# Optimization experiments

Hardware: AMD Instinct MI355X
Metric: run time of the kernel (lower is better)

The kernel has to match this reference:

```python
import jax, jax.numpy as jnp
import numpy as np

NH, HD = 12, 64          # heads, head dim (d_model=768)
SC = HD ** -0.5          # both Attention and CA_Attention use head_dim**-0.5


def patchify(x, p1, p2):
    # 'b c (h p1) (w p2) -> b (h w) (p1 p2 c)'
    B, C, H, W = x.shape
    h, w = H // p1, W // p2
    x = x.reshape(B, C, h, p1, w, p2).transpose(0, 2, 4, 3, 5, 1)  # b h w p1 p2 c
    return x.reshape(B, h * w, p1 * p2 * C)


def unpatchify(x, h, w, p1, p2, c):
    # 'b (h w) (p1 p2 c) -> b c (h p1) (w p2)'
    B = x.shape[0]
    x = x.reshape(B, h, w, p1, p2, c).transpose(0, 5, 1, 3, 2, 4)
    return x.reshape(B, c, h * p1, w * p2)


def ln(x, g, b):
    m = x.mean(-1, keepdims=True)
    v = ((x - m) ** 2).mean(-1, keepdims=True)
    return (x - m) / jnp.sqrt(v + 1e-5) * g + b


def setup_inputs() -> dict:
    key = jax.random.key(0)
    specs = [
        ('img_feats', (2, 32, 112, 112, 80)), ('txt', (2, 77, 768)),
        ('pe_w_ax', (1120, 768)), ('pe_b_ax', (768,)),
        ('pe_w_sag', (1120, 768)), ('pe_b_sag', (768,)),
        ('pe_w_cor', (1568, 768)), ('pe_b_cor', (768,)),
        ('pos_ax', (1, 256, 768)), ('pos_sag', (1, 256, 768)), ('pos_cor', (1, 256, 768)),
        ('qw', (768, 768)), ('kw', (768, 768)), ('vw', (768, 768)),
        ('pw', (768, 768)), ('pb', (768,)),
        ('caq_w', (768, 768)), ('caq_b', (768,)), ('cak_w', (768, 768)), ('cak_b', (768,)),
        ('cav_w', (768, 768)), ('cav_b', (768,)), ('cao_w', (768, 768)), ('cao_b', (768,)),
        ('mlp_w1', (768, 3072)), ('mlp_b1', (3072,)), ('mlp_w2', (3072, 768)), ('mlp_b2', (768,)),
        ('ow_ax', (768, 1120)), ('ob_ax', (1120,)),
        ('ow_sag', (768, 1120)), ('ob_sag', (1120,)),
        ('ow_cor', (768, 1568)), ('ob_cor', (1568,)),
    ]
    big = {'img_feats', 'txt', 'pos_ax', 'pos_sag', 'pos_cor'}
    out = {}
    for k, (n, s) in zip(jax.random.split(key, len(specs)), specs):
        scale = 1.0 if n in big else 0.02
        out[n] = jax.random.normal(k, s, jnp.float32) * scale
    out['view_w'] = jnp.ones((3,), jnp.float32)
    for n in ('n1_g', 'n2_g', 'n3_g'):
        out[n] = jnp.ones((768,), jnp.float32)
    for n in ('n1_b', 'n2_b', 'n3_b'):
        out[n] = jnp.zeros((768,), jnp.float32)
    return out


def reference(img_feats, txt, pe_w_ax, pe_b_ax, pe_w_sag, pe_b_sag, pe_w_cor, pe_b_cor,
              pos_ax, pos_sag, pos_cor, view_w, qw, kw, vw, pw, pb,
              caq_w, caq_b, cak_w, cak_b, cav_w, cav_b, cao_w, cao_b,
              n1_g, n1_b, n2_g, n2_b, n3_g, n3_b,
              mlp_w1, mlp_b1, mlp_w2, mlp_b2,
              ow_ax, ob_ax, ow_sag, ob_sag, ow_cor, ob_cor):

    def img_attn(t):
        B, N, C = t.shape
        q = (t @ qw).reshape(B, N, NH, HD)
        k = (t @ kw).reshape(B, N, NH, HD)
        v = (t @ vw).reshape(B, N, NH, HD)
        a = jax.nn.softmax(jnp.einsum('bnkc,bmkc->bknm', q, k) * SC, axis=-1)
        x = jnp.einsum('bknm,bmkc->bnkc', a, v).reshape(B, N, C)
        return x @ pw + pb

    def ca_attn(t, im):
        B, T, _ = t.shape
        N = im.shape[1]
        qh = (t @ caq_w + caq_b).reshape(B, T, NH, HD).transpose(0, 2, 1, 3)
        kh = (im @ cak_w + cak_b).reshape(B, N, NH, HD).transpose(0, 2, 1, 3)
        vh = (im @ cav_w + cav_b).reshape(B, N, NH, HD).transpose(0, 2, 1, 3)
        a = jax.nn.softmax(jnp.einsum('bhid,bhjd->bhij', qh, kh) * SC, axis=-1)
        # faithful to original einsum 'b h i j, b h j d -> b h j d' (sums over i)
        o = jnp.einsum('bhij,bhjd->bhjd', a, vh)
        o = o.transpose(0, 2, 1, 3).reshape(B, N, NH * HD)
        return o @ cao_w + cao_b

    def branch(v2d, pe_w, pe_b, pos, ow, ob, p1, p2):
        B, C, H, W = v2d.shape
        h, w = H // p1, W // p2
        q = patchify(v2d, p1, p2) @ pe_w + pe_b + pos
        q = ln(q, n1_g, n1_b)
        q = q + img_attn(q)
        q = ln(q, n2_g, n2_b)
        x = q + ca_attn(txt, q)
        x = x + (jax.nn.gelu(ln(x, n3_g, n3_b) @ mlp_w1 + mlp_b1, approximate=False) @ mlp_w2 + mlp_b2)
        return unpatchify(x @ ow + ob, h, w, p1, p2, C)

    # adaptive_avg_pool3d to size-1 along one axis == mean over that axis
    ax = img_feats.mean(2)    # (B,C,H,W)
    sag = img_feats.mean(3)   # (B,C,D,W)
    cor = img_feats.mean(4)   # (B,C,D,H)
    oax = branch(ax, pe_w_ax, pe_b_ax, pos_ax, ow_ax, ob_ax, 7, 5)
    osag = branch(sag, pe_w_sag, pe_b_sag, pos_sag, ow_sag, ob_sag, 7, 5)
    ocor = branch(cor, pe_w_cor, pe_b_cor, pos_cor, ow_cor, ob_cor, 7, 7)
    v3 = (view_w[0] * oax[:, :, None] + view_w[1] * osag[:, :, :, None]
          + view_w[2] * ocor[:, :, :, :, None])
    return img_feats + v3
```

## Files before the change

kernel.cpp:

```cpp
#include <hip/hip_runtime.h>
#include <math.h>

typedef __attribute__((ext_vector_type(8))) short s8;
typedef __attribute__((ext_vector_type(4))) float f4;
typedef unsigned short u16;

__device__ inline u16 f2bf(float f) {
    unsigned u = __float_as_uint(f);
    u += 0x7fffu + ((u >> 16) & 1u);
    return (u16)(u >> 16);
}
__device__ inline float bf2f(u16 x) {
    return __uint_as_float(((unsigned)x) << 16);
}

__global__ __launch_bounds__(256) void mean3_k(const float* __restrict__ img,
                                               float* __restrict__ axp,
                                               float* __restrict__ sag,
                                               float* __restrict__ cor) {
    __shared__ float sl[112*81];
    int blk = blockIdx.x;
    int dc = blk & 15, bc = blk >> 4;
    int d0 = dc * 7;
    int t = threadIdx.x;
    f4 axr[9];
    #pragma unroll
    for (int k = 0; k < 9; ++k) axr[k] = (f4){0.f,0.f,0.f,0.f};
    const float* base = img + (size_t)bc * 1003520 + (size_t)d0 * 8960;
    for (int sidx = 0; sidx < 7; ++sidx) {
        const f4* sp = reinterpret_cast<const f4*>(base + (size_t)sidx * 8960);
        #pragma unroll
        for (int k = 0; k < 9; ++k) {
            int q = t + k * 256;
            if (q < 2240) {
                f4 v = sp[q];
                axr[k] += v;
                int h = q / 20, w4 = q % 20;
                float* row = &sl[h * 81 + w4 * 4];
                row[0] = v[0]; row[1] = v[1]; row[2] = v[2]; row[3] = v[3];
            }
        }
        __syncthreads();
        if (t < 112) {
            float acc = 0.f;
            #pragma unroll 8
            for (int w = 0; w < 80; ++w) acc += sl[t * 81 + w];
            cor[((size_t)bc * 112 + d0 + sidx) * 112 + t] = acc * (1.f / 80.f);
        } else if (t < 192) {
            int w = t - 112;
            float acc = 0.f;
            #pragma unroll 8
            for (int h = 0; h < 112; ++h) acc += sl[h * 81 + w];
            sag[((size_t)bc * 112 + d0 + sidx) * 80 + w] = acc * (1.f / 112.f);
        }
        __syncthreads();
    }
    float* axo = axp + ((size_t)dc * 64 + bc) * 8960;
    #pragma unroll
    for (int k = 0; k < 9; ++k) {
        int q = t + k * 256;
        if (q < 2240) *reinterpret_cast<f4*>(axo + q * 4) = axr[k];
    }
}

__global__ void axred_k(const float* __restrict__ axp, float* __restrict__ ax) {
    int idx = blockIdx.x * 256 + threadIdx.x;
    if (idx >= 143360) return;
    f4 s = (f4){0.f,0.f,0.f,0.f};
    #pragma unroll
    for (int i = 0; i < 16; ++i)
        s += *reinterpret_cast<const f4*>(axp + (size_t)i * 573440 + (size_t)idx * 4);
    s *= (1.f / 112.f);
    *reinterpret_cast<f4*>(ax + (size_t)idx * 4) = s;
}

struct TT {
    const float* in[16];
    u16* out[16];
    int K[16];
    int N[16];
    int start[16];
};

__global__ __launch_bounds__(256) void transp_all(TT tab) {
    __shared__ float tl[32][33];
    int bid = blockIdx.x;
    int e = 0;
    #pragma unroll
    for (int i = 1; i < 16; ++i) if (bid >= tab.start[i]) e = i;
    const float* in = tab.in[e];
    u16* out = tab.out[e];
    int K = tab.K[e], N = tab.N[e];
    int tid = bid - tab.start[e];
    int nt = N >> 5;
    int k0 = (tid / nt) * 32, n0 = (tid % nt) * 32;
    int t = threadIdx.x;
    int r = t >> 5, c = t & 31;
    #pragma unroll
    for (int i = 0; i < 4; ++i) tl[r + i*8][c] = in[(long)(k0 + r + i*8)*N + n0 + c];
    __syncthreads();
    #pragma unroll
    for (int i = 0; i < 4; ++i) out[(long)(n0 + r + i*8)*K + k0 + c] = f2bf(tl[c][r + i*8]);
}

__global__ void misc_k(const float* __restrict__ txt, u16* __restrict__ txtb,
                       const float* __restrict__ cak_b, const float* __restrict__ cav_b,
                       float* __restrict__ kvb) {
    int idx = blockIdx.x*256 + threadIdx.x;
    if (idx < 118272) { txtb[idx] = f2bf(txt[idx]); return; }
    int i2 = idx - 118272;
    if (i2 < 768) kvb[i2] = cak_b[i2];
    else if (i2 < 1536) kvb[i2] = cav_b[i2 - 768];
}

__global__ __launch_bounds__(256) void patchify3_k(const float* __restrict__ m_ax,
                                                   const float* __restrict__ m_sag,
                                                   const float* __restrict__ m_cor,
                                                   u16* __restrict__ P0, u16* __restrict__ P1,
                                                   u16* __restrict__ P2) {
    __shared__ float sl[32][113];
    int br = blockIdx.y;
    int X = blockIdx.x;
    int b = X / 112, rem = X % 112;
    int hh = rem / 7, pp1 = rem % 7;
    const float* src; u16* dst; int Wt, p2, PD;
    if (br == 0)      { src = m_ax;  dst = P0; Wt = 80;  p2 = 5; PD = 1120; }
    else if (br == 1) { src = m_sag; dst = P1; Wt = 80;  p2 = 5; PD = 1120; }
    else              { src = m_cor; dst = P2; Wt = 112; p2 = 7; PD = 1568; }
    int t = threadIdx.x;
    int row = hh*7 + pp1;
    int wq = Wt >> 2;
    for (int i = t; i < 32*wq; i += 256) {
        int c = i / wq, w4 = i % wq;
        float4 v = *reinterpret_cast<const float4*>(
            src + ((size_t)(b*32 + c)*112 + row)*Wt + w4*4);
        sl[c][w4*4+0] = v.x; sl[c][w4*4+1] = v.y; sl[c][w4*4+2] = v.z; sl[c][w4*4+3] = v.w;
    }
    __syncthreads();
    int tot = 16 * p2 * 32;
    for (int o = t; o < tot; o += 256) {
        int ww = o / (p2*32), rest = o % (p2*32);
        int pp2 = rest >> 5, c = rest & 31;
        dst[((size_t)(b*256 + hh*16 + ww))*PD + (pp1*p2 + pp2)*32 + c]
            = f2bf(sl[c][ww*p2 + pp2]);
    }
}

__device__ inline void load_tile(const u16* __restrict__ P, int ld, int nrows, int K,
                                 int r0, int k0, int t, s8 v[4]) {
    #pragma unroll
    for (int i = 0; i < 4; ++i) {
        int chunk = t + i*256;
        int row = chunk >> 4, c8 = (chunk & 15) * 8;
        s8 x;
        #pragma unroll
        for (int q = 0; q < 8; ++q) x[q] = 0;
        if (r0 + row < nrows && k0 + c8 < K)
            x = *reinterpret_cast<const s8*>(P + (long)(r0 + row)*ld + k0 + c8);
        v[i] = x;
    }
}
__device__ inline void write_tile(u16 (*S)[136], int t, const s8 v[4]) {
    #pragma unroll
    for (int i = 0; i < 4; ++i) {
        int chunk = t + i*256;
        *reinterpret_cast<s8*>(&S[chunk >> 4][(chunk & 15)*8]) = v[i];
    }
}
__device__ inline void mfma_tile(const u16 (*As)[136], const u16 (*Bs)[136],
                                 int wr, int wc, int lane, f4 acc[2][2]) {
    int lrow = lane & 15;
    #pragma unroll
    for (int kh = 0; kh < 4; ++kh) {
        int lk = kh*32 + (lane >> 4) * 8;
        s8 af0 = *reinterpret_cast<const s8*>(&As[wr*32 + lrow][lk]);
        s8 af1 = *reinterpret_cast<const s8*>(&As[wr*32 + 16 + lrow][lk]);
        s8 bg0 = *reinterpret_cast<const s8*>(&Bs[wc*32 + lrow][lk]);
        s8 bg1 = *reinterpret_cast<const s8*>(&Bs[wc*32 + 16 + lrow][lk]);
        acc[0][0] = __builtin_amdgcn_mfma_f32_16x16x32_bf16(af0, bg0, acc[0][0], 0, 0, 0);
        acc[0][1] = __builtin_amdgcn_mfma_f32_16x16x32_bf16(af0, bg1, acc[0][1], 0, 0, 0);
        acc[1][0] = __builtin_amdgcn_mfma_f32_16x16x32_bf16(af1, bg0, acc[1][0], 0, 0, 0);
        acc[1][1] = __builtin_amdgcn_mfma_f32_16x16x32_bf16(af1, bg1, acc[1][1], 0, 0, 0);
    }
}

__global__ __launch_bounds__(256) void gemm_bf(
    const u16* __restrict__ A, const u16* __restrict__ Bt,
    float* __restrict__ Cf, u16* __restrict__ Cb,
    int M, int N, int K, int lda, int ldb, int ldc,
    const float* __restrict__ bias, const float* __restrict__ resid,
    int act, float cscale, int mode)
{
    __shared__ u16 As[2][64][136];
    __shared__ u16 Bs[2][64][136];
    const u16* Ab = A;
    const u16* Bb = Bt;
    long coff = 0;
    int z = blockIdx.z;
    if (mode == 1) {
        long o = (long)(z / 12) * 256 * lda + (long)(z % 12) * 64;
        Ab += o; Bb += o; coff = (long)z * 256 * ldc;
    } else if (mode == 2) {
        Ab += (long)z * 65536; Bb += (long)z * 16384;
        coff = (long)(z / 12) * 256 * ldc + (long)(z % 12) * 64;
    } else if (mode == 3) {
        int rowblk = z / 12, h = z % 12;
        Ab += (long)(rowblk & 1) * 77 * lda + (long)h * 64;
        Bb += (long)rowblk * 256 * ldb + (long)h * 64;
        coff = (long)z * 77 * 256;
    }
    int t = threadIdx.x;
    int m0 = blockIdx.y * 64, n0 = blockIdx.x * 64;
    int wave = t >> 6, lane = t & 63;
    int wr = wave >> 1, wc = wave & 1;
    f4 acc[2][2];
    #pragma unroll
    for (int m = 0; m < 2; ++m)
        #pragma unroll
        for (int n = 0; n < 2; ++n)
            #pragma unroll
            for (int r = 0; r < 4; ++r) acc[m][n][r] = 0.f;
    int nk = (K + 127) >> 7;
    s8 pa[4], pbv[4];
    load_tile(Ab, lda, M, K, m0, 0, t, pa);
    load_tile(Bb, ldb, N, K, n0, 0, t, pbv);
    write_tile(As[0], t, pa);
    write_tile(Bs[0], t, pbv);
    __syncthreads();
    for (int kt = 0; kt < nk; ++kt) {
        int cur = kt & 1;
        if (kt + 1 < nk) {
            load_tile(Ab, lda, M, K, m0, (kt+1) << 7, t, pa);
            load_tile(Bb, ldb, N, K, n0, (kt+1) << 7, t, pbv);
        }
        mfma_tile(As[cur], Bs[cur], wr, wc, lane, acc);
        if (kt + 1 < nk) {
            write_tile(As[cur^1], t, pa);
            write_tile(Bs[cur^1], t, pbv);
        }
        __syncthreads();
    }
    #pragma unroll
    for (int m = 0; m < 2; ++m) {
        int rbase = m0 + wr*32 + m*16 + (lane >> 4) * 4;
        #pragma unroll
        for (int n = 0; n < 2; ++n) {
            int col = n0 + wc*32 + n*16 + (lane & 15);
            if (col >= N) continue;
            #pragma unroll
            for (int r = 0; r < 4; ++r) {
                int row = rbase + r;
                if (row >= M) continue;
                float v = acc[m][n][r];
                if (bias)  v += bias[col];
                if (resid) v += resid[(long)row * ldc + col];
                if (act == 1) v = 0.5f * v * (1.0f + erff(v * 0.70710678118654752f));
                v *= cscale;
                long ci = coff + (long)row * ldc + col;
                if (Cf) Cf[ci] = v;
                if (Cb) Cb[ci] = f2bf(v);
            }
        }
    }
}

__global__ __launch_bounds__(256) void gemm_big(
    const u16* __restrict__ A, const u16* __restrict__ Bt,
    u16* __restrict__ Cb, u16* __restrict__ vt,
    int N, int K,
    const float* __restrict__ bias, int act)
{
    __shared__ u16 As[2][128][72];
    __shared__ u16 Bs[2][128][72];
    int t = threadIdx.x;
    int m0 = blockIdx.y * 128, n0 = blockIdx.x * 128;
    int wave = t >> 6, lane = t & 63;
    int wr = wave >> 1, wc = wave & 1;
    f4 acc[4][4];
    #pragma unroll
    for (int m = 0; m < 4; ++m)
        #pragma unroll
        for (int n = 0; n < 4; ++n)
            #pragma unroll
            for (int r = 0; r < 4; ++r) acc[m][n][r] = 0.f;
    int nk = K >> 6;
    s8 pa[4], pbv[4];
    #pragma unroll
    for (int i = 0; i < 4; ++i) {
        int chunk = t + i*256;
        pa[i]  = *reinterpret_cast<const s8*>(A  + (long)(m0 + (chunk>>3))*K + (chunk&7)*8);
        pbv[i] = *reinterpret_cast<const s8*>(Bt + (long)(n0 + (chunk>>3))*K + (chunk&7)*8);
// ... 1 lines not shown
    #pragma unroll
    for (int i = 0; i < 4; ++i) {
        int chunk = t + i*256;
        *reinterpret_cast<s8*>(&As[0][chunk>>3][(chunk&7)*8]) = pa[i];
        *reinterpret_cast<s8*>(&Bs[0][chunk>>3][(chunk&7)*8]) = pbv[i];
    }
    __syncthreads();
    for (int kt = 0; kt < nk; ++kt) {
        int cur = kt & 1;
        if (kt + 1 < nk) {
            int k0 = (kt+1) << 6;
            #pragma unroll
            for (int i = 0; i < 4; ++i) {
                int chunk = t + i*256;
                pa[i]  = *reinterpret_cast<const s8*>(A  + (long)(m0 + (chunk>>3))*K + k0 + (chunk&7)*8);
                pbv[i] = *reinterpret_cast<const s8*>(Bt + (long)(n0 + (chunk>>3))*K + k0 + (chunk&7)*8);
            }
        }
        #pragma unroll
        for (int kh = 0; kh < 2; ++kh) {
            int lk = kh*32 + (lane >> 4) * 8;
            int lr = lane & 15;
            s8 af[4], bf[4];
            #pragma unroll
            for (int m = 0; m < 4; ++m)
                af[m] = *reinterpret_cast<const s8*>(&As[cur][wr*64 + m*16 + lr][lk]);
            #pragma unroll
            for (int n = 0; n < 4; ++n)
                bf[n] = *reinterpret_cast<const s8*>(&Bs[cur][wc*64 + n*16 + lr][lk]);
            #pragma unroll
            for (int m = 0; m < 4; ++m)
                #pragma unroll
                for (int n = 0; n < 4; ++n)
                    acc[m][n] = __builtin_amdgcn_mfma_f32_16x16x32_bf16(af[m], bf[n], acc[m][n], 0, 0, 0);
        }
        if (kt + 1 < nk) {
            #pragma unroll
            for (int i = 0; i < 4; ++i) {
                int chunk = t + i*256;
                *reinterpret_cast<s8*>(&As[cur^1][chunk>>3][(chunk&7)*8]) = pa[i];
                *reinterpret_cast<s8*>(&Bs[cur^1][chunk>>3][(chunk&7)*8]) = pbv[i];
            }
        }
        __syncthreads();
    }
    #pragma unroll
    for (int m = 0; m < 4; ++m) {
        int rbase = m0 + wr*64 + m*16 + (lane >> 4) * 4;
        #pragma unroll
        for (int n = 0; n < 4; ++n) {
            int col = n0 + wc*64 + n*16 + (lane & 15);
            #pragma unroll
            for (int r = 0; r < 4; ++r) {
                int row = rbase + r;
                float v = acc[m][n][r];
                if (bias) v += bias[col];
                if (act == 1) v = 0.5f * v * (1.0f + erff(v * 0.70710678118654752f));
                u16 b = f2bf(v);
                Cb[(long)row * N + col] = b;
                if (vt && col >= 1536) {
                    int z = (row >> 8) * 12 + ((col - 1536) >> 6);
                    vt[((long)z * 64 + (col & 63)) * 256 + (row & 255)] = b;
                }
            }
        }
    }
}

struct PeDesc {
    const u16* A[3];
    const u16* Bt[3];
    const float* bias[3];
    const float* pos[3];
    int K[3];
};

__global__ __launch_bounds__(256) void gemm_pe(PeDesc d, float* __restrict__ C) {
    __shared__ u16 As[2][64][136];
    __shared__ u16 Bs[2][64][136];
    int z = blockIdx.z;
    const u16* Ab = d.A[z];
    const u16* Bb = d.Bt[z];
    const float* bias = d.bias[z];
    const float* pos = d.pos[z];
    int K = d.K[z];
    int t = threadIdx.x;
    int m0 = blockIdx.y * 64, n0 = blockIdx.x * 64;
    int wave = t >> 6, lane = t & 63;
    int wr = wave >> 1, wc = wave & 1;
    f4 acc[2][2];
    #pragma unroll
    for (int m = 0; m < 2; ++m)
        #pragma unroll
        for (int n = 0; n < 2; ++n)
            #pragma unroll
            for (int r = 0; r < 4; ++r) acc[m][n][r] = 0.f;
    int nk = (K + 127) >> 7;
    s8 pa[4], pbv[4];
    load_tile(Ab, K, 512, K, m0, 0, t, pa);
    load_tile(Bb, K, 768, K, n0, 0, t, pbv);
    write_tile(As[0], t, pa);
    write_tile(Bs[0], t, pbv);
    __syncthreads();
    for (int kt = 0; kt < nk; ++kt) {
        int cur = kt & 1;
        if (kt + 1 < nk) {
            load_tile(Ab, K, 512, K, m0, (kt+1) << 7, t, pa);
            load_tile(Bb, K, 768, K, n0, (kt+1) << 7, t, pbv);
        }
        mfma_tile(As[cur], Bs[cur], wr, wc, lane, acc);
        if (kt + 1 < nk) {
            write_tile(As[cur^1], t, pa);
            write_tile(Bs[cur^1], t, pbv);
        }
        __syncthreads();
    }
    float* Cz = C + (long)z * 512 * 768;
    #pragma unroll
    for (int m = 0; m < 2; ++m) {
        int rbase = m0 + wr*32 + m*16 + (lane >> 4) * 4;
        #pragma unroll
        for (int n = 0; n < 2; ++n) {
            int col = n0 + wc*32 + n*16 + (lane & 15);
            #pragma unroll
            for (int r = 0; r < 4; ++r) {
                int row = rbase + r;
                float v = acc[m][n][r] + bias[col] + pos[(long)(row & 255)*768 + col];
                Cz[(long)row * 768 + col] = v;
            }
        }
    }
}

struct OwDesc {
    const u16* Bt[3];
    float* C[3];
    const float* bias[3];
    int N[3];
};

__global__ __launch_bounds__(256) void gemm_ow(OwDesc d, const u16* __restrict__ A) {
    int z = blockIdx.z;
    int N = d.N[z];
    int n0 = blockIdx.x * 64;
    if (n0 >= N) return;
    __shared__ u16 As[2][64][136];
    __shared__ u16 Bs[2][64][136];
    const u16* Ab = A + (long)z * 512 * 768;
    const u16* Bb = d.Bt[z];
    int t = threadIdx.x;
    int m0 = blockIdx.y * 64;
    int wave = t >> 6, lane = t & 63;
    int wr = wave >> 1, wc = wave & 1;
    f4 acc[2][2];
    #pragma unroll
    for (int m = 0; m < 2; ++m)
        #pragma unroll
        for (int n = 0; n < 2; ++n)
            #pragma unroll
            for (int r = 0; r < 4; ++r) acc[m][n][r] = 0.f;
    s8 pa[4], pbv[4];
// ... 42 lines not shown
    int row = blockIdx.x;
    const float* x = in + (size_t)row * N;
    int t = threadIdx.x;
    float v0 = x[t], v1 = x[t+256], v2 = x[t+512];
    float s = v0+v1+v2, s2 = v0*v0+v1*v1+v2*v2;
    #pragma unroll
    for (int off = 32; off > 0; off >>= 1) { s += __shfl_down(s, off); s2 += __shfl_down(s2, off); }
    __shared__ float red[8];
    int wid = t >> 6, lane = t & 63;
    if (lane == 0) { red[wid] = s; red[wid+4] = s2; }
    __syncthreads();
    if (t == 0) {
        float S = red[0]+red[1]+red[2]+red[3];
        float S2 = red[4]+red[5]+red[6]+red[7];
        float mean = S * (1.f/N);
        float var = S2 * (1.f/N) - mean*mean;
        red[0] = mean; red[1] = rsqrtf(var + 1e-5f);
    }
    __syncthreads();
    float mean = red[0], rstd = red[1];
    float y0 = (v0-mean)*rstd*g[t]     + bta[t];
    float y1 = (v1-mean)*rstd*g[t+256] + bta[t+256];
    float y2 = (v2-mean)*rstd*g[t+512] + bta[t+512];
    if (outf) {
        float* y = outf + (size_t)row * N;
        y[t] = y0; y[t+256] = y1; y[t+512] = y2;
    }
    if (outb) {
        u16* y = outb + (size_t)row * N;
        y[t] = f2bf(y0); y[t+256] = f2bf(y1); y[t+512] = f2bf(y2);
    }
}

__global__ __launch_bounds__(256) void softmax_k(const float* __restrict__ S,
                                                 u16* __restrict__ P) {
    int row = blockIdx.x*4 + (threadIdx.x >> 6);
    int lane = threadIdx.x & 63;
    const float4 v = *reinterpret_cast<const float4*>(S + (long)row*256 + lane*4);
    float m = fmaxf(fmaxf(v.x, v.y), fmaxf(v.z, v.w));
    #pragma unroll
    for (int o = 32; o; o >>= 1) m = fmaxf(m, __shfl_xor(m, o));
    float p0 = __expf(v.x - m), p1 = __expf(v.y - m), p2 = __expf(v.z - m), p3 = __expf(v.w - m);
    float l = p0 + p1 + p2 + p3;
    #pragma unroll
    for (int o = 32; o; o >>= 1) l += __shfl_xor(l, o);
    float inv = 1.f / l;
    unsigned b0 = f2bf(p0*inv), b1 = f2bf(p1*inv), b2 = f2bf(p2*inv), b3 = f2bf(p3*inv);
    uint2 pk; pk.x = b0 | (b1 << 16); pk.y = b2 | (b3 << 16);
    *reinterpret_cast<uint2*>(P + (long)row*256 + lane*4) = pk;
}

__global__ __launch_bounds__(256) void ca_k(const float* __restrict__ S2,
                                            const u16* __restrict__ KVHb,
                                            u16* __restrict__ O) {
    __shared__ float sl[4*256];
    __shared__ float wj[256];
    int bh = blockIdx.x;
    int rowblk = bh / 12, h = bh % 12;
    int t = threadIdx.x;
    int w = t >> 6, lane = t & 63;
    float wacc[4] = {0.f, 0.f, 0.f, 0.f};
    for (int i = w; i < 77; i += 4) {
        const float4 v = *reinterpret_cast<const float4*>(S2 + ((long)bh*77 + i)*256 + lane*4);
        float m = fmaxf(fmaxf(v.x, v.y), fmaxf(v.z, v.w));
        #pragma unroll
        for (int o = 32; o; o >>= 1) m = fmaxf(m, __shfl_xor(m, o));
        float p0 = __expf(v.x - m), p1 = __expf(v.y - m), p2 = __expf(v.z - m), p3 = __expf(v.w - m);
        float l = p0 + p1 + p2 + p3;
        #pragma unroll
        for (int o = 32; o; o >>= 1) l += __shfl_xor(l, o);
        float inv = 1.f / l;
        wacc[0] += p0*inv; wacc[1] += p1*inv; wacc[2] += p2*inv; wacc[3] += p3*inv;
    }
    #pragma unroll
    for (int k = 0; k < 4; ++k) sl[w*256 + lane*4 + k] = wacc[k];
    __syncthreads();
    wj[t] = sl[t] + sl[256 + t] + sl[512 + t] + sl[768 + t];
    __syncthreads();
    int d = t & 63;
    #pragma unroll 4
    for (int it = 0; it < 64; ++it) {
        int j = it*4 + (t >> 6);
        long row = (long)rowblk*256 + j;
        float vh = bf2f(KVHb[row*1536 + 768 + h*64 + d]);
        O[row*768 + h*64 + d] = f2bf(wj[j] * vh);
    }
}

__global__ void unpatch3_k(const float* __restrict__ Y0, const float* __restrict__ Y1,
                           const float* __restrict__ Y2, const float* __restrict__ vw,
                           float* __restrict__ Aax, float* __restrict__ Asag,
                           float* __restrict__ Acor) {
    int idx = blockIdx.x*256 + threadIdx.x;
    if (idx >= 1949696) return;
    const float* y; float* A; float wt; int Wd, p2, PD, p;
    if (idx < 573440)       { y = Y0; A = Aax;  wt = vw[0]; Wd = 80;  p2 = 5; PD = 1120; p = idx; }
    else if (idx < 1146880) { y = Y1; A = Asag; wt = vw[1]; Wd = 80;  p2 = 5; PD = 1120; p = idx - 573440; }
    else                    { y = Y2; A = Acor; wt = vw[2]; Wd = 112; p2 = 7; PD = 1568; p = idx - 1146880; }
    int w = p % Wd; int r = p / Wd;
    int h = r % 112; r /= 112;
    int c = r % 32; int b = r / 32;
    int src = (b*256 + (h/7)*16 + (w/p2))*PD + ((h%7)*p2 + (w%p2))*32 + c;
    A[p] = wt * y[src];
}

__global__ __launch_bounds__(256) void final_k(const float* __restrict__ img,
                                               const float* __restrict__ Aax,
                                               const float* __restrict__ Asag,
                                               const float* __restrict__ Acor,
                                               float* __restrict__ out) {
    int blk = blockIdx.x;
    int bc = blk / 112;
    const float4* ip = reinterpret_cast<const float4*>(img + (size_t)blk * 8960);
    const float4* ap = reinterpret_cast<const float4*>(Aax + (size_t)bc * 8960);
    const float4* sp = reinterpret_cast<const float4*>(Asag + (size_t)blk * 80);
    const float*  cp = Acor + (size_t)blk * 112;
    float4* op = reinterpret_cast<float4*>(out + (size_t)blk * 8960);
    int t = threadIdx.x;
// ... 29 lines not shown
    const float* cak_w = (const float*)d_in[18];
    const float* cak_b = (const float*)d_in[19];
    const float* cav_w = (const float*)d_in[20];
    const float* cav_b = (const float*)d_in[21];
    const float* cao_w = (const float*)d_in[22];
    const float* cao_b = (const float*)d_in[23];
    const float* mlp_w1 = (const float*)d_in[24];
    const float* mlp_b1 = (const float*)d_in[25];
    const float* mlp_w2 = (const float*)d_in[26];
    const float* mlp_b2 = (const float*)d_in[27];
    const float* ow[3] = {(const float*)d_in[28], (const float*)d_in[30], (const float*)d_in[32]};
    const float* ob[3] = {(const float*)d_in[29], (const float*)d_in[31], (const float*)d_in[33]};
    const float* view_w = (const float*)d_in[34];
    const float* n_g[3] = {(const float*)d_in[35], (const float*)d_in[36], (const float*)d_in[37]};
    const float* n_b[3] = {(const float*)d_in[38], (const float*)d_in[39], (const float*)d_in[40]};

    unsigned char* sb = (unsigned char*)d_out;
    size_t off = 0;
    auto B = [&](size_t bytes) -> void* {
        void* p = sb + off; off += (bytes + 511) & ~(size_t)511; return p;
    };
    u16* qkvT  = (u16*)B((size_t)2304*768*2);
    u16* pwT   = (u16*)B(768*768*2);
    u16* caqT  = (u16*)B(768*768*2);
    u16* cakvT = (u16*)B((size_t)1536*768*2);
    u16* caoT  = (u16*)B(768*768*2);
    u16* mlp1T = (u16*)B((size_t)3072*768*2);
    u16* mlp2T = (u16*)B((size_t)768*3072*2);
    u16* peT[3]; peT[0] = (u16*)B((size_t)768*1120*2); peT[1] = (u16*)B((size_t)768*1120*2); peT[2] = (u16*)B((size_t)768*1568*2);
    u16* owT[3]; owT[0] = (u16*)B((size_t)1120*768*2); owT[1] = (u16*)B((size_t)1120*768*2); owT[2] = (u16*)B((size_t)1568*768*2);
    u16* txtb = (u16*)B(154*768*2);
    float* kvb = (float*)B(1536*4);
    float* axp   = (float*)B((size_t)16*573440*4);
    float* m_ax  = (float*)B(573440*4);
    float* m_sag = (float*)B(573440*4);
    float* m_cor = (float*)B(802816*4);
    u16* P0 = (u16*)B((size_t)512*1120*2);
    u16* P1 = (u16*)B((size_t)512*1120*2);
    u16* P2 = (u16*)B((size_t)512*1568*2);
    float* X0  = (float*)B((size_t)1536*768*4);
    float* X1f = (float*)B((size_t)1536*768*4);
    float* X2  = (float*)B((size_t)1536*768*4);
    float* X3f = (float*)B((size_t)1536*768*4);
    float* X4  = (float*)B((size_t)1536*768*4);
    u16* X1b = (u16*)B((size_t)1536*768*2);
    u16* X3b = (u16*)B((size_t)1536*768*2);
    u16* X5b = (u16*)B((size_t)1536*768*2);
    u16* X6b = (u16*)B((size_t)1536*768*2);
    u16* QKVb = (u16*)B((size_t)1536*2304*2);
    u16* Obf = (u16*)B((size_t)1536*768*2);
    u16* Vt  = (u16*)B((size_t)72*64*256*2);
    u16* Hb  = (u16*)B((size_t)1536*3072*2);
    float* S  = (float*)B((size_t)72*256*256*4);
    u16* Pat = (u16*)B((size_t)72*256*256*2);
    u16* KVHb = (u16*)B((size_t)1536*1536*2);
    u16* QHb  = (u16*)B((size_t)154*768*2);
    float* S2 = (float*)B((size_t)72*77*256*4);
    float* Y[3];
    Y[0] = (float*)B(573440*4);
    Y[1] = (float*)B(573440*4);
    Y[2] = (float*)B(802816*4);

    float* ws = (float*)d_ws;
    float* Aax  = ws;
    float* Asag = ws + 573440;
    float* Acor = ws + 1146880;

    TT tab;
    {
        const float* ins[16] = {qw, kw, vw_attn, pw, caq_w, cak_w, cav_w, cao_w,
                                mlp_w1, mlp_w2, pe_w[0], pe_w[1], pe_w[2], ow[0], ow[1], ow[2]};
        u16* outs[16] = {qkvT, qkvT + 768*768, qkvT + 2*768*768, pwT, caqT, cakvT,
                         cakvT + 768*768, caoT, mlp1T, mlp2T, peT[0], peT[1], peT[2],
                         owT[0], owT[1], owT[2]};
        int Ks[16] = {768,768,768,768,768,768,768,768, 768,3072, 1120,1120,1568, 768,768,768};
        int Ns[16] = {768,768,768,768,768,768,768,768, 3072,768, 768,768,768, 1120,1120,1568};
        int st = 0;
        for (int i = 0; i < 16; ++i) {
            tab.in[i] = ins[i]; tab.out[i] = outs[i]; tab.K[i] = Ks[i]; tab.N[i] = Ns[i];
            tab.start[i] = st;
            st += (Ks[i] >> 5) * (Ns[i] >> 5);
        }
        transp_all<<<st, 256, 0, stream>>>(tab);
    }
    misc_k<<<468, 256, 0, stream>>>(txt, txtb, cak_b, cav_b, kvb);

    mean3_k<<<1024, 256, 0, stream>>>(img, axp, m_sag, m_cor);
    axred_k<<<560, 256, 0, stream>>>(axp, m_ax);
    patchify3_k<<<dim3(224,3), 256, 0, stream>>>(m_ax, m_sag, m_cor, P0, P1, P2);

    auto gemm = [&](const u16* A, const u16* Bt, float* Cf, u16* Cb,
                    int M, int N, int K, int lda, int ldb, int ldc,
                    const float* bias, const float* resid,
                    int act, float cscale, int mode, int batch) {
        dim3 g((N+63)/64, (M+63)/64, batch);
        gemm_bf<<<g, 256, 0, stream>>>(A, Bt, Cf, Cb, M, N, K, lda, ldb, ldc,
                                       bias, resid, act, cscale, mode);
    };

    gemm(txtb, caqT, nullptr, QHb, 154, 768, 768, 768, 768, 768,
         caq_b, nullptr, 0, 1.f, 0, 1);

    {
        PeDesc d;
        d.A[0] = P0; d.A[1] = P1; d.A[2] = P2;
        d.Bt[0] = peT[0]; d.Bt[1] = peT[1]; d.Bt[2] = peT[2];
        d.bias[0] = pe_b[0]; d.bias[1] = pe_b[1]; d.bias[2] = pe_b[2];
        d.pos[0] = pos[0]; d.pos[1] = pos[1]; d.pos[2] = pos[2];
        d.K[0] = 1120; d.K[1] = 1120; d.K[2] = 1568;
        gemm_pe<<<dim3(12,8,3), 256, 0, stream>>>(d, X0);
    }

    ln_k<<<1536, 256, 0, stream>>>(X0, X1f, X1b, n_g[0], n_b[0]);
    gemm_big<<<dim3(18,12), 256, 0, stream>>>(X1b, qkvT, QKVb, Vt, 2304, 768, nullptr, 0);
    gemm(QKVb, QKVb + 768, S, nullptr, 256, 256, 64, 2304, 2304, 256,
         nullptr, nullptr, 0, 0.125f, 1, 72);
    softmax_k<<<4608, 256, 0, stream>>>(S, Pat);
    gemm(Pat, Vt, nullptr, Obf, 256, 64, 256, 256, 256, 768,
         nullptr, nullptr, 0, 1.f, 2, 72);
    gemm(Obf, pwT, X2, nullptr, 1536, 768, 768, 768, 768, 768, pb, X1f, 0, 1.f, 0, 1);
    ln_k<<<1536, 256, 0, stream>>>(X2, X3f, X3b, n_g[1], n_b[1]);
    gemm_big<<<dim3(12,12), 256, 0, stream>>>(X3b, cakvT, KVHb, nullptr, 1536, 768, kvb, 0);
    gemm(QHb, KVHb, S2, nullptr, 77, 256, 64, 768, 1536, 256,
         nullptr, nullptr, 0, 0.125f, 3, 72);
    ca_k<<<72, 256, 0, stream>>>(S2, KVHb, Obf);
    gemm(Obf, caoT, X4, nullptr, 1536, 768, 768, 768, 768, 768, cao_b, X3f, 0, 1.f, 0, 1);
    ln_k<<<1536, 256, 0, stream>>>(X4, nullptr, X5b, n_g[2], n_b[2]);
    gemm_big<<<dim3(24,12), 256, 0, stream>>>(X5b, mlp1T, Hb, nullptr, 3072, 768, mlp_b1, 1);
    gemm(Hb, mlp2T, nullptr, X6b, 1536, 768, 3072, 3072, 3072, 768, mlp_b2, X4, 0, 1.f, 0, 1);
    {
        OwDesc d;
        d.Bt[0] = owT[0]; d.Bt[1] = owT[1]; d.Bt[2] = owT[2];
        d.C[0] = Y[0]; d.C[1] = Y[1]; d.C[2] = Y[2];
        d.bias[0] = ob[0]; d.bias[1] = ob[1]; d.bias[2] = ob[2];
        d.N[0] = 1120; d.N[1] = 1120; d.N[2] = 1568;
        gemm_ow<<<dim3(25,8,3), 256, 0, stream>>>(d, X6b);
    }

    unpatch3_k<<<7616, 256, 0, stream>>>(Y[0], Y[1], Y[2], view_w, Aax, Asag, Acor);
    final_k<<<7168, 256, 0, stream>>>(img, Aax, Asag, Acor, (float*)d_out);
}
```

Baseline: 489.0 us.

## Fuse self- and cross-attention into single kernels and merge small launches

Replaces the batched QK^T GEMM, separate softmax kernel, and PV GEMM with one attn_k kernel that keeps scores in registers and probabilities in shared memory. It also fuses the cross-attention score GEMM with its softmax and column-sum into ca_fused. The axial mean reduction is folded into patchify, and the text query projection is folded into the patch-embedding GEMM launch. Together these remove the fp32 score and probability buffers and several launches. In exchange, attn_k runs only 144 blocks with large register and LDS use, which may limit occupancy.

New measurement: 451.5 us. -7.7%, faster.

```diff
diff --git a/kernel.cpp b/kernel.cpp
--- a/kernel.cpp
+++ b/kernel.cpp
@@ -13,6 +13,7 @@
 __device__ inline float bf2f(u16 x) {
     return __uint_as_float(((unsigned)x) << 16);
 }
+#define MFMA16(a, b, c) __builtin_amdgcn_mfma_f32_16x16x32_bf16(a, b, c, 0, 0, 0)
 
 __global__ __launch_bounds__(256) void mean3_k(const float* __restrict__ img,
                                                float* __restrict__ axp,
@@ -63,17 +64,6 @@
     }
 }
 
-__global__ void axred_k(const float* __restrict__ axp, float* __restrict__ ax) {
-    int idx = blockIdx.x * 256 + threadIdx.x;
-    if (idx >= 143360) return;
-    f4 s = (f4){0.f,0.f,0.f,0.f};
-    #pragma unroll
-    for (int i = 0; i < 16; ++i)
-        s += *reinterpret_cast<const f4*>(axp + (size_t)i * 573440 + (size_t)idx * 4);
-    s *= (1.f / 112.f);
-    *reinterpret_cast<f4*>(ax + (size_t)idx * 4) = s;
-}
-
 struct TT {
     const float* in[16];
     u16* out[16];
@@ -113,7 +103,7 @@
     else if (i2 < 1536) kvb[i2] = cav_b[i2 - 768];
 }
 
-__global__ __launch_bounds__(256) void patchify3_k(const float* __restrict__ m_ax,
+__global__ __launch_bounds__(256) void patchify3_k(const float* __restrict__ axp,
                                                    const float* __restrict__ m_sag,
                                                    const float* __restrict__ m_cor,
                                                    u16* __restrict__ P0, u16* __restrict__ P1,
@@ -124,17 +114,30 @@
     int b = X / 112, rem = X % 112;
     int hh = rem / 7, pp1 = rem % 7;
     const float* src; u16* dst; int Wt, p2, PD;
-    if (br == 0)      { src = m_ax;  dst = P0; Wt = 80;  p2 = 5; PD = 1120; }
-    else if (br == 1) { src = m_sag; dst = P1; Wt = 80;  p2 = 5; PD = 1120; }
-    else              { src = m_cor; dst = P2; Wt = 112; p2 = 7; PD = 1568; }
+    if (br == 0)      { src = nullptr; dst = P0; Wt = 80;  p2 = 5; PD = 1120; }
+    else if (br == 1) { src = m_sag;   dst = P1; Wt = 80;  p2 = 5; PD = 1120; }
+    else              { src = m_cor;   dst = P2; Wt = 112; p2 = 7; PD = 1568; }
     int t = threadIdx.x;
     int row = hh*7 + pp1;
     int wq = Wt >> 2;
-    for (int i = t; i < 32*wq; i += 256) {
-        int c = i / wq, w4 = i % wq;
-        float4 v = *reinterpret_cast<const float4*>(
-            src + ((size_t)(b*32 + c)*112 + row)*Wt + w4*4);
-        sl[c][w4*4+0] = v.x; sl[c][w4*4+1] = v.y; sl[c][w4*4+2] = v.z; sl[c][w4*4+3] = v.w;
+    if (br == 0) {
+        for (int i = t; i < 32*20; i += 256) {
+            int c = i / 20, w4 = i % 20;
+            f4 s = (f4){0.f,0.f,0.f,0.f};
+            size_t base = ((size_t)(b*32 + c)*112 + row)*80 + w4*4;
+            #pragma unroll
+            for (int p = 0; p < 16; ++p)
+                s += *reinterpret_cast<const f4*>(axp + (size_t)p*573440 + base);
+            s *= (1.f/112.f);
+            sl[c][w4*4+0] = s[0]; sl[c][w4*4+1] = s[1]; sl[c][w4*4+2] = s[2]; sl[c][w4*4+3] = s[3];
+        }
+    } else {
+        for (int i = t; i < 32*wq; i += 256) {
+            int c = i / wq, w4 = i % wq;
+            float4 v = *reinterpret_cast<const float4*>(
+                src + ((size_t)(b*32 + c)*112 + row)*Wt + w4*4);
+            sl[c][w4*4+0] = v.x; sl[c][w4*4+1] = v.y; sl[c][w4*4+2] = v.z; sl[c][w4*4+3] = v.w;
+        }
     }
     __syncthreads();
     int tot = 16 * p2 * 32;
@@ -177,38 +180,22 @@
         s8 af1 = *reinterpret_cast<const s8*>(&As[wr*32 + 16 + lrow][lk]);
         s8 bg0 = *reinterpret_cast<const s8*>(&Bs[wc*32 + lrow][lk]);
         s8 bg1 = *reinterpret_cast<const s8*>(&Bs[wc*32 + 16 + lrow][lk]);
-        acc[0][0] = __builtin_amdgcn_mfma_f32_16x16x32_bf16(af0, bg0, acc[0][0], 0, 0, 0);
-        acc[0][1] = __builtin_amdgcn_mfma_f32_16x16x32_bf16(af0, bg1, acc[0][1], 0, 0, 0);
-        acc[1][0] = __builtin_amdgcn_mfma_f32_16x16x32_bf16(af1, bg0, acc[1][0], 0, 0, 0);
-        acc[1][1] = __builtin_amdgcn_mfma_f32_16x16x32_bf16(af1, bg1, acc[1][1], 0, 0, 0);
+        acc[0][0] = MFMA16(af0, bg0, acc[0][0]);
+        acc[0][1] = MFMA16(af0, bg1, acc[0][1]);
+        acc[1][0] = MFMA16(af1, bg0, acc[1][0]);
+        acc[1][1] = MFMA16(af1, bg1, acc[1][1]);
     }
 }
 
 __global__ __launch_bounds__(256) void gemm_bf(
     const u16* __restrict__ A, const u16* __restrict__ Bt,
     float* __restrict__ Cf, u16* __restrict__ Cb,
-    int M, int N, int K, int lda, int ldb, int ldc,
+    int M, int N, int K,
     const float* __restrict__ bias, const float* __restrict__ resid,
-    int act, float cscale, int mode)
+    int act)
 {
     __shared__ u16 As[2][64][136];
     __shared__ u16 Bs[2][64][136];
-    const u16* Ab = A;
-    const u16* Bb = Bt;
-    long coff = 0;
-    int z = blockIdx.z;
-    if (mode == 1) {
-        long o = (long)(z / 12) * 256 * lda + (long)(z % 12) * 64;
-        Ab += o; Bb += o; coff = (long)z * 256 * ldc;
-    } else if (mode == 2) {
-        Ab += (long)z * 65536; Bb += (long)z * 16384;
-        coff = (long)(z / 12) * 256 * ldc + (long)(z % 12) * 64;
-    } else if (mode == 3) {
-        int rowblk = z / 12, h = z % 12;
-        Ab += (long)(rowblk & 1) * 77 * lda + (long)h * 64;
-        Bb += (long)rowblk * 256 * ldb + (long)h * 64;
-        coff = (long)z * 77 * 256;
-    }
     int t = threadIdx.x;
     int m0 = blockIdx.y * 64, n0 = blockIdx.x * 64;
     int wave = t >> 6, lane = t & 63;
@@ -222,16 +209,16 @@
             for (int r = 0; r < 4; ++r) acc[m][n][r] = 0.f;
     int nk = (K + 127) >> 7;
     s8 pa[4], pbv[4];
-    load_tile(Ab, lda, M, K, m0, 0, t, pa);
-    load_tile(Bb, ldb, N, K, n0, 0, t, pbv);
+    load_tile(A, K, M, K, m0, 0, t, pa);
+    load_tile(Bt, K, N, K, n0, 0, t, pbv);
     write_tile(As[0], t, pa);
     write_tile(Bs[0], t, pbv);
     __syncthreads();
     for (int kt = 0; kt < nk; ++kt) {
         int cur = kt & 1;
         if (kt + 1 < nk) {
-            load_tile(Ab, lda, M, K, m0, (kt+1) << 7, t, pa);
-            load_tile(Bb, ldb, N, K, n0, (kt+1) << 7, t, pbv);
+            load_tile(A, K, M, K, m0, (kt+1) << 7, t, pa);
+            load_tile(Bt, K, N, K, n0, (kt+1) << 7, t, pbv);
         }
         mfma_tile(As[cur], Bs[cur], wr, wc, lane, acc);
         if (kt + 1 < nk) {
@@ -253,10 +240,9 @@
                 if (row >= M) continue;
                 float v = acc[m][n][r];
                 if (bias)  v += bias[col];
-                if (resid) v += resid[(long)row * ldc + col];
+                if (resid) v += resid[(long)row * N + col];
                 if (act == 1) v = 0.5f * v * (1.0f + erff(v * 0.70710678118654752f));
-                v *= cscale;
-                long ci = coff + (long)row * ldc + col;
+                long ci = (long)row * N + col;
                 if (Cf) Cf[ci] = v;
                 if (Cb) Cb[ci] = f2bf(v);
             }
@@ -324,7 +310,7 @@
             for (int m = 0; m < 4; ++m)
                 #pragma unroll
                 for (int n = 0; n < 4; ++n)
-                    acc[m][n] = __builtin_amdgcn_mfma_f32_16x16x32_bf16(af[m], bf[n], acc[m][n], 0, 0, 0);
+                    acc[m][n] = MFMA16(af[m], bf[n], acc[m][n]);
         }
         if (kt + 1 < nk) {
             #pragma unroll
@@ -360,24 +346,27 @@
 }
 
 struct PeDesc {
-    const u16* A[3];
-    const u16* Bt[3];
-    const float* bias[3];
-    const float* pos[3];
-    int K[3];
+    const u16* A[4];
+    const u16* Bt[4];
+    const float* bias[4];
+    const float* pos[4];
+    int K[4];
+    int M[4];
 };
 
-__global__ __launch_bounds__(256) void gemm_pe(PeDesc d, float* __restrict__ C) {
+__global__ __launch_bounds__(256) void gemm_pe(PeDesc d, float* __restrict__ C,
+                                               u16* __restrict__ QHb) {
+    int z = blockIdx.z;
+    int M = d.M[z], K = d.K[z];
+    int m0 = blockIdx.y * 64, n0 = blockIdx.x * 64;
+    if (m0 >= M) return;
     __shared__ u16 As[2][64][136];
     __shared__ u16 Bs[2][64][136];
-    int z = blockIdx.z;
     const u16* Ab = d.A[z];
     const u16* Bb = d.Bt[z];
     const float* bias = d.bias[z];
     const float* pos = d.pos[z];
-    int K = d.K[z];
-    int t = threadIdx.x;
-    int m0 = blockIdx.y * 64, n0 = blockIdx.x * 64;
+    int t = threadIdx.x;
     int wave = t >> 6, lane = t & 63;
     int wr = wave >> 1, wc = wave & 1;
     f4 acc[2][2];
@@ -389,7 +378,7 @@
             for (int r = 0; r < 4; ++r) acc[m][n][r] = 0.f;
     int nk = (K + 127) >> 7;
     s8 pa[4], pbv[4];
-    load_tile(Ab, K, 512, K, m0, 0, t, pa);
+    load_tile(Ab, K, M, K, m0, 0, t, pa);
     load_tile(Bb, K, 768, K, n0, 0, t, pbv);
     write_tile(As[0], t, pa);
     write_tile(Bs[0], t, pbv);
@@ -397,7 +386,7 @@
     for (int kt = 0; kt < nk; ++kt) {
         int cur = kt & 1;
         if (kt + 1 < nk) {
-            load_tile(Ab, K, 512, K, m0, (kt+1) << 7, t, pa);
+            load_tile(Ab, K, M, K, m0, (kt+1) << 7, t, pa);
             load_tile(Bb, K, 768, K, n0, (kt+1) << 7, t, pbv);
         }
         mfma_tile(As[cur], Bs[cur], wr, wc, lane, acc);
@@ -407,7 +396,6 @@
         }
         __syncthreads();
     }
-    float* Cz = C + (long)z * 512 * 768;
     #pragma unroll
     for (int m = 0; m < 2; ++m) {
         int rbase = m0 + wr*32 + m*16 + (lane >> 4) * 4;
@@ -417,8 +405,14 @@
             #pragma unroll
             for (int r = 0; r < 4; ++r) {
                 int row = rbase + r;
-                float v = acc[m][n][r] + bias[col] + pos[(long)(row & 255)*768 + col];
-                Cz[(long)row * 768 + col] = v;
+                if (row >= M) continue;
+                float v = acc[m][n][r] + bias[col];
+                if (z < 3) {
+                    v += pos[(long)(row & 255)*768 + col];
+                    C[((long)z*512 + row) * 768 + col] = v;
+                } else {
+                    QHb[(long)row * 768 + col] = f2bf(v);
+                }
             }
         }
     }
@@ -527,50 +521,212 @@
     }
 }
 
-__global__ __launch_bounds__(256) void softmax_k(const float* __restrict__ S,
-                                                 u16* __restrict__ P) {
-    int row = blockIdx.x*4 + (threadIdx.x >> 6);
-    int lane = threadIdx.x & 63;
-    const float4 v = *reinterpret_cast<const float4*>(S + (long)row*256 + lane*4);
-    float m = fmaxf(fmaxf(v.x, v.y), fmaxf(v.z, v.w));
-    #pragma unroll
-    for (int o = 32; o; o >>= 1) m = fmaxf(m, __shfl_xor(m, o));
-    float p0 = __expf(v.x - m), p1 = __expf(v.y - m), p2 = __expf(v.z - m), p3 = __expf(v.w - m);
-    float l = p0 + p1 + p2 + p3;
-    #pragma unroll
-    for (int o = 32; o; o >>= 1) l += __shfl_xor(l, o);
-    float inv = 1.f / l;
-    unsigned b0 = f2bf(p0*inv), b1 = f2bf(p1*inv), b2 = f2bf(p2*inv), b3 = f2bf(p3*inv);
-    uint2 pk; pk.x = b0 | (b1 << 16); pk.y = b2 | (b3 << 16);
-    *reinterpret_cast<uint2*>(P + (long)row*256 + lane*4) = pk;
-}
-
-__global__ __launch_bounds__(256) void ca_k(const float* __restrict__ S2,
-                                            const u16* __restrict__ KVHb,
-                                            u16* __restrict__ O) {
-    __shared__ float sl[4*256];
-    __shared__ float wj[256];
+__global__ __launch_bounds__(256) void attn_k(const u16* __restrict__ QKV,
+                                              const u16* __restrict__ Vt,
+                                              u16* __restrict__ O) {
+    __shared__ u16 Ks[256][72];
+    __shared__ u16 Ps[128][264];
+    __shared__ u16 Vs[64][264];
+    int zz = blockIdx.x;
+    int bh = zz >> 1, half = zz & 1;
+    int bb = bh / 12, h = bh % 12;
+    long qrow0 = (long)bb*256 + half*128;
+    int hcol = h*64;
+    int t = threadIdx.x;
+    int wave = t >> 6, lane = t & 63;
+    int lr = lane & 15, lg = lane >> 4;
+    #pragma unroll
+    for (int i = 0; i < 8; ++i) {
+        int chunk = t + i*256;
+        int row = chunk >> 3, c8 = (chunk & 7)*8;
+        *reinterpret_cast<s8*>(&Ks[row][c8]) =
+            *reinterpret_cast<const s8*>(QKV + ((long)bb*256 + row)*2304 + 768 + hcol + c8);
+    }
+    #pragma unroll
+    for (int i = 0; i < 8; ++i) {
+        int chunk = t + i*256;
+        int d = chunk >> 5, j8 = (chunk & 31)*8;
+        *reinterpret_cast<s8*>(&Vs[d][j8]) =
+            *reinterpret_cast<const s8*>(Vt + (long)bh*16384 + (long)d*256 + j8);
+    }
+    __syncthreads();
+    f4 acc[2][16];
+    #pragma unroll
+    for (int m = 0; m < 2; ++m)
+        #pragma unroll
+        for (int n = 0; n < 16; ++n)
+            #pragma unroll
+            for (int r = 0; r < 4; ++r) acc[m][n][r] = 0.f;
+    #pragma unroll
+    for (int kh = 0; kh < 2; ++kh) {
+        s8 af0 = *reinterpret_cast<const s8*>(QKV + (qrow0 + wave*32 + lr)*2304 + hcol + kh*32 + lg*8);
+        s8 af1 = *reinterpret_cast<const s8*>(QKV + (qrow0 + wave*32 + 16 + lr)*2304 + hcol + kh*32 + lg*8);
+        #pragma unroll
+        for (int n = 0; n < 16; ++n) {
+            s8 bf = *reinterpret_cast<const s8*>(&Ks[n*16 + lr][kh*32 + lg*8]);
+            acc[0][n] = MFMA16(af0, bf, acc[0][n]);
+            acc[1][n] = MFMA16(af1, bf, acc[1][n]);
+        }
+    }
+    #pragma unroll
+    for (int m = 0; m < 2; ++m)
+        #pragma unroll
+        for (int r = 0; r < 4; ++r) {
+            float mx = -1e30f;
+            #pragma unroll
+            for (int n = 0; n < 16; ++n) mx = fmaxf(mx, acc[m][n][r]);
+            #pragma unroll
+            for (int o = 8; o; o >>= 1) mx = fmaxf(mx, __shfl_xor(mx, o));
+            float l = 0.f;
+            float p[16];
+            #pragma unroll
+            for (int n = 0; n < 16; ++n) {
+                p[n] = __expf((acc[m][n][r] - mx) * 0.125f);
+                l += p[n];
+            }
+            #pragma unroll
+            for (int o = 8; o; o >>= 1) l += __shfl_xor(l, o);
+            float inv = 1.f / l;
+            int prow = wave*32 + m*16 + lg*4 + r;
+            #pragma unroll
+            for (int n = 0; n < 16; ++n)
+                Ps[prow][n*16 + lr] = f2bf(p[n] * inv);
+        }
+    __syncthreads();
+    f4 o2[2][4];
+    #pragma unroll
+    for (int m = 0; m < 2; ++m)
+        #pragma unroll
+        for (int n = 0; n < 4; ++n)
+            #pragma unroll
+            for (int r = 0; r < 4; ++r) o2[m][n][r] = 0.f;
+    #pragma unroll
+    for (int kh = 0; kh < 8; ++kh) {
+        s8 pf0 = *reinterpret_cast<const s8*>(&Ps[wave*32 + lr][kh*32 + lg*8]);
+        s8 pf1 = *reinterpret_cast<const s8*>(&Ps[wave*32 + 16 + lr][kh*32 + lg*8]);
+        #pragma unroll
+        for (int n = 0; n < 4; ++n) {
+            s8 vf = *reinterpret_cast<const s8*>(&Vs[n*16 + lr][kh*32 + lg*8]);
+            o2[0][n] = MFMA16(pf0, vf, o2[0][n]);
+            o2[1][n] = MFMA16(pf1, vf, o2[1][n]);
+        }
+    }
+    #pragma unroll
+    for (int m = 0; m < 2; ++m)
+        #pragma unroll
+        for (int n = 0; n < 4; ++n)
+            #pragma unroll
+            for (int r = 0; r < 4; ++r)
+                O[(qrow0 + wave*32 + m*16 + lg*4 + r)*768 + hcol + n*16 + lr] = f2bf(o2[m][n][r]);
+}
+
+__global__ __launch_bounds__(256) void ca_fused(const u16* __restrict__ QHb,
+                                                const u16* __restrict__ KVHb,
+                                                u16* __restrict__ O) {
+    __shared__ u16 QHs[80][72];
+    __shared__ u16 KHs[256][72];
+    __shared__ float rmax[80][4];
+    __shared__ float rsum[80][4];
+    __shared__ float Wj[256];
     int bh = blockIdx.x;
     int rowblk = bh / 12, h = bh % 12;
-    int t = threadIdx.x;
-    int w = t >> 6, lane = t & 63;
-    float wacc[4] = {0.f, 0.f, 0.f, 0.f};
-    for (int i = w; i < 77; i += 4) {
-        const float4 v = *reinterpret_cast<const float4*>(S2 + ((long)bh*77 + i)*256 + lane*4);
-        float m = fmaxf(fmaxf(v.x, v.y), fmaxf(v.z, v.w));
-        #pragma unroll
-        for (int o = 32; o; o >>= 1) m = fmaxf(m, __shfl_xor(m, o));
-        float p0 = __expf(v.x - m), p1 = __expf(v.y - m), p2 = __expf(v.z - m), p3 = __expf(v.w - m);
-        float l = p0 + p1 + p2 + p3;
-        #pragma unroll
-        for (int o = 32; o; o >>= 1) l += __shfl_xor(l, o);
-        float inv = 1.f / l;
-        wacc[0] += p0*inv; wacc[1] += p1*inv; wacc[2] += p2*inv; wacc[3] += p3*inv;
-    }
-    #pragma unroll
-    for (int k = 0; k < 4; ++k) sl[w*256 + lane*4 + k] = wacc[k];
-    __syncthreads();
-    wj[t] = sl[t] + sl[256 + t] + sl[512 + t] + sl[768 + t];
+    int bsel = rowblk & 1;
+    int t = threadIdx.x;
+    int wave = t >> 6, lane = t & 63;
+    int lr = lane & 15, lg = lane >> 4;
+    #pragma unroll
+    for (int i = 0; i < 3; ++i) {
+        int chunk = t + i*256;
+        if (chunk < 640) {
+            int row = chunk >> 3, c8 = (chunk & 7)*8;
+            s8 v;
+            #pragma unroll
+            for (int q = 0; q < 8; ++q) v[q] = 0;
+            if (row < 77)
+                v = *reinterpret_cast<const s8*>(QHb + ((long)(bsel*77 + row))*768 + h*64 + c8);
+            *reinterpret_cast<s8*>(&QHs[row][c8]) = v;
+        }
+    }
+    #pragma unroll
+    for (int i = 0; i < 8; ++i) {
+        int chunk = t + i*256;
+        int row = chunk >> 3, c8 = (chunk & 7)*8;
+        *reinterpret_cast<s8*>(&KHs[row][c8]) =
+            *reinterpret_cast<const s8*>(KVHb + ((long)rowblk*256 + row)*1536 + h*64 + c8);
+    }
+    __syncthreads();
+    f4 acc[5][4];
+    #pragma unroll
+    for (int m = 0; m < 5; ++m)
+        #pragma unroll
+        for (int n = 0; n < 4; ++n)
+            #pragma unroll
+            for (int r = 0; r < 4; ++r) acc[m][n][r] = 0.f;
+    #pragma unroll
+    for (int kh = 0; kh < 2; ++kh) {
+        s8 af[5], bf[4];
+        #pragma unroll
+        for (int m = 0; m < 5; ++m)
+            af[m] = *reinterpret_cast<const s8*>(&QHs[m*16 + lr][kh*32 + lg*8]);
+        #pragma unroll
+        for (int n = 0; n < 4; ++n)
+            bf[n] = *reinterpret_cast<const s8*>(&KHs[wave*64 + n*16 + lr][kh*32 + lg*8]);
+        #pragma unroll
+        for (int m = 0; m < 5; ++m)
+            #pragma unroll
+            for (int n = 0; n < 4; ++n)
+                acc[m][n] = MFMA16(af[m], bf[n], acc[m][n]);
+    }
+    #pragma unroll
+    for (int m = 0; m < 5; ++m)
+        #pragma unroll
+        for (int r = 0; r < 4; ++r) {
+            float mx = -1e30f;
+            #pragma unroll
+            for (int n = 0; n < 4; ++n) mx = fmaxf(mx, acc[m][n][r]);
+            #pragma unroll
+            for (int o = 8; o; o >>= 1) mx = fmaxf(mx, __shfl_xor(mx, o));
+            if (lr == 0) rmax[m*16 + lg*4 + r][wave] = mx;
+        }
+    __syncthreads();
+    #pragma unroll
+    for (int m = 0; m < 5; ++m)
+        #pragma unroll
+        for (int r = 0; r < 4; ++r) {
+            int i = m*16 + lg*4 + r;
+            float mi = fmaxf(fmaxf(rmax[i][0], rmax[i][1]), fmaxf(rmax[i][2], rmax[i][3]));
+            float s = 0.f;
+            #pragma unroll
+            for (int n = 0; n < 4; ++n) s += __expf((acc[m][n][r] - mi) * 0.125f);
+            #pragma unroll
+            for (int o = 8; o; o >>= 1) s += __shfl_xor(s, o);
+            if (lr == 0) rsum[i][wave] = s;
+        }
+    __syncthreads();
+    float wn[4] = {0.f, 0.f, 0.f, 0.f};
+    #pragma unroll
+    for (int m = 0; m < 5; ++m)
+        #pragma unroll
+        for (int r = 0; r < 4; ++r) {
+            int i = m*16 + lg*4 + r;
+            if (i < 77) {
+                float mi = fmaxf(fmaxf(rmax[i][0], rmax[i][1]), fmaxf(rmax[i][2], rmax[i][3]));
+                float li = rsum[i][0] + rsum[i][1] + rsum[i][2] + rsum[i][3];
+                float inv = 1.f / li;
+                #pragma unroll
+                for (int n = 0; n < 4; ++n)
+                    wn[n] += __expf((acc[m][n][r] - mi) * 0.125f) * inv;
+            }
+        }
+    #pragma unroll
+    for (int n = 0; n < 4; ++n) {
+        wn[n] += __shfl_xor(wn[n], 16);
+        wn[n] += __shfl_xor(wn[n], 32);
+    }
+    if (lane < 16) {
+        #pragma unroll
+        for (int n = 0; n < 4; ++n) Wj[wave*64 + n*16 + lr] = wn[n];
+    }
     __syncthreads();
     int d = t & 63;
     #pragma unroll 4
@@ -578,7 +734,7 @@
         int j = it*4 + (t >> 6);
         long row = (long)rowblk*256 + j;
         float vh = bf2f(KVHb[row*1536 + 768 + h*64 + d]);
-        O[row*768 + h*64 + d] = f2bf(wj[j] * vh);
+        O[row*768 + h*64 + d] = f2bf(Wj[j] * vh);
     }
 }
 
@@ -674,7 +830,6 @@
     u16* txtb = (u16*)B(154*768*2);
     float* kvb = (float*)B(1536*4);
     float* axp   = (float*)B((size_t)16*573440*4);
-    float* m_ax  = (float*)B(573440*4);
     float* m_sag = (float*)B(573440*4);
     float* m_cor = (float*)B(802816*4);
     u16* P0 = (u16*)B((size_t)512*1120*2);
@@ -693,11 +848,8 @@
     u16* Obf = (u16*)B((size_t)1536*768*2);
     u16* Vt  = (u16*)B((size_t)72*64*256*2);
     u16* Hb  = (u16*)B((size_t)1536*3072*2);
-    float* S  = (float*)B((size_t)72*256*256*4);
-    u16* Pat = (u16*)B((size_t)72*256*256*2);
     u16* KVHb = (u16*)B((size_t)1536*1536*2);
     u16* QHb  = (u16*)B((size_t)154*768*2);
-    float* S2 = (float*)B((size_t)72*77*256*4);
     float* Y[3];
     Y[0] = (float*)B(573440*4);
     Y[1] = (float*)B(573440*4);
@@ -728,48 +880,36 @@
     misc_k<<<468, 256, 0, stream>>>(txt, txtb, cak_b, cav_b, kvb);
 
     mean3_k<<<1024, 256, 0, stream>>>(img, axp, m_sag, m_cor);
-    axred_k<<<560, 256, 0, stream>>>(axp, m_ax);
-    patchify3_k<<<dim3(224,3), 256, 0, stream>>>(m_ax, m_sag, m_cor, P0, P1, P2);
+    patchify3_k<<<dim3(224,3), 256, 0, stream>>>(axp, m_sag, m_cor, P0, P1, P2);
 
     auto gemm = [&](const u16* A, const u16* Bt, float* Cf, u16* Cb,
-                    int M, int N, int K, int lda, int ldb, int ldc,
-                    const float* bias, const float* resid,
-                    int act, float cscale, int mode, int batch) {
-        dim3 g((N+63)/64, (M+63)/64, batch);
-        gemm_bf<<<g, 256, 0, stream>>>(A, Bt, Cf, Cb, M, N, K, lda, ldb, ldc,
-                                       bias, resid, act, cscale, mode);
+                    int M, int N, int K, const float* bias, const float* resid, int act) {
+        dim3 g((N+63)/64, (M+63)/64, 1);
+        gemm_bf<<<g, 256, 0, stream>>>(A, Bt, Cf, Cb, M, N, K, bias, resid, act);
     };
-
-    gemm(txtb, caqT, nullptr, QHb, 154, 768, 768, 768, 768, 768,
-         caq_b, nullptr, 0, 1.f, 0, 1);
 
     {
         PeDesc d;
-        d.A[0] = P0; d.A[1] = P1; d.A[2] = P2;
-        d.Bt[0] = peT[0]; d.Bt[1] = peT[1]; d.Bt[2] = peT[2];
-        d.bias[0] = pe_b[0]; d.bias[1] = pe_b[1]; d.bias[2] = pe_b[2];
-        d.pos[0] = pos[0]; d.pos[1] = pos[1]; d.pos[2] = pos[2];
-        d.K[0] = 1120; d.K[1] = 1120; d.K[2] = 1568;
-        gemm_pe<<<dim3(12,8,3), 256, 0, stream>>>(d, X0);
+        d.A[0] = P0; d.A[1] = P1; d.A[2] = P2; d.A[3] = txtb;
+        d.Bt[0] = peT[0]; d.Bt[1] = peT[1]; d.Bt[2] = peT[2]; d.Bt[3] = caqT;
+        d.bias[0] = pe_b[0]; d.bias[1] = pe_b[1]; d.bias[2] = pe_b[2]; d.bias[3] = caq_b;
+        d.pos[0] = pos[0]; d.pos[1] = pos[1]; d.pos[2] = pos[2]; d.pos[3] = nullptr;
+        d.K[0] = 1120; d.K[1] = 1120; d.K[2] = 1568; d.K[3] = 768;
+        d.M[0] = 512; d.M[1] = 512; d.M[2] = 512; d.M[3] = 154;
+        gemm_pe<<<dim3(12,8,4), 256, 0, stream>>>(d, X0, QHb);
     }
 
     ln_k<<<1536, 256, 0, stream>>>(X0, X1f, X1b, n_g[0], n_b[0]);
     gemm_big<<<dim3(18,12), 256, 0, stream>>>(X1b, qkvT, QKVb, Vt, 2304, 768, nullptr, 0);
-    gemm(QKVb, QKVb + 768, S, nullptr, 256, 256, 64, 2304, 2304, 256,
-         nullptr, nullptr, 0, 0.125f, 1, 72);
-    softmax_k<<<4608, 256, 0, stream>>>(S, Pat);
-    gemm(Pat, Vt, nullptr, Obf, 256, 64, 256, 256, 256, 768,
-         nullptr, nullptr, 0, 1.f, 2, 72);
-    gemm(Obf, pwT, X2, nullptr, 1536, 768, 768, 768, 768, 768, pb, X1f, 0, 1.f, 0, 1);
+    attn_k<<<144, 256, 0, stream>>>(QKVb, Vt, Obf);
+    gemm(Obf, pwT, X2, nullptr, 1536, 768, 768, pb, X1f, 0);
     ln_k<<<1536, 256, 0, stream>>>(X2, X3f, X3b, n_g[1], n_b[1]);
     gemm_big<<<dim3(12,12), 256, 0, stream>>>(X3b, cakvT, KVHb, nullptr, 1536, 768, kvb, 0);
-    gemm(QHb, KVHb, S2, nullptr, 77, 256, 64, 768, 1536, 256,
-         nullptr, nullptr, 0, 0.125f, 3, 72);
-    ca_k<<<72, 256, 0, stream>>>(S2, KVHb, Obf);
-    gemm(Obf, caoT, X4, nullptr, 1536, 768, 768, 768, 768, 768, cao_b, X3f, 0, 1.f, 0, 1);
+    ca_fused<<<72, 256, 0, stream>>>(QHb, KVHb, Obf);
+    gemm(Obf, caoT, X4, nullptr, 1536, 768, 768, cao_b, X3f, 0);
     ln_k<<<1536, 256, 0, stream>>>(X4, nullptr, X5b, n_g[2], n_b[2]);
     gemm_big<<<dim3(24,12), 256, 0, stream>>>(X5b, mlp1T, Hb, nullptr, 3072, 768, mlp_b1, 1);
-    gemm(Hb, mlp2T, nullptr, X6b, 1536, 768, 3072, 3072, 3072, 768, mlp_b2, X4, 0, 1.f, 0, 1);
+    gemm(Hb, mlp2T, nullptr, X6b, 1536, 768, 3072, mlp_b2, X4, 0);
     {
         OwDesc d;
         d.Bt[0] = owT[0]; d.Bt[1] = owT[1]; d.Bt[2] = owT[2];
```
